# Kernel optimization log

Hardware: AMD Instinct MI355X
Metric: run time of the kernel (lower is better)

Reference implementation:

```python
import jax, jax.numpy as jnp
import numpy as np

EMBED_DIM = 1024
HEADS = 16
ATTN_NORM = 64  # scale divisor: score / sqrt(ATTN_NORM)


def setup_inputs() -> dict:
    key = jax.random.key(0)
    ks = jax.random.split(key, 12)
    B, S, E = 2, 2048, EMBED_DIM
    s = 1.0 / np.sqrt(E)
    inp = {
        "q": jax.random.normal(ks[0], (B, S, E), jnp.float32),
        "k": jax.random.normal(ks[1], (B, S, E), jnp.float32),
        "v": jax.random.normal(ks[2], (B, S, E), jnp.float32),
        "mask": jnp.zeros((B, 1, 1, S), dtype=bool),
        "Wq": jax.random.normal(ks[3], (E, E), jnp.float32) * s,
        "bq": jnp.zeros((E,), jnp.float32),
        "Wk": jax.random.normal(ks[4], (E, E), jnp.float32) * s,
        "bk": jnp.zeros((E,), jnp.float32),
        "Wv": jax.random.normal(ks[5], (E, E), jnp.float32) * s,
        "bv": jnp.zeros((E,), jnp.float32),
        "Wo": jax.random.normal(ks[6], (E, E), jnp.float32) * s,
        "bo": jnp.zeros((E,), jnp.float32),
    }
    return inp


def reference(q, k, v, mask, Wq, bq, Wk, bk, Wv, bv, Wo, bo):
    B, S, E = q.shape
    H = HEADS
    D = E // H
    residual = q
    # QKV projections (torch Linear: x @ W.T + b)
    qh = (q @ Wq.T + bq).reshape(B, S, H, D).transpose(0, 2, 1, 3)  # [B,H,S,D]
    kh = (k @ Wk.T + bk).reshape(B, S, H, D).transpose(0, 2, 1, 3)
    vh = (v @ Wv.T + bv).reshape(B, S, H, D).transpose(0, 2, 1, 3)
    # scaled dot-product attention with boolean mask -> -inf
    score = jnp.einsum("bhqd,bhkd->bhqk", qh, kh) / jnp.sqrt(jnp.asarray(ATTN_NORM, qh.dtype))
    score = jnp.where(mask, -jnp.inf, score)
    attn = jax.nn.softmax(score, axis=-1)
    out = jnp.einsum("bhqk,bhkd->bhqd", attn, vh)
    out = out.transpose(0, 2, 1, 3).reshape(B, S, E)
    # output projection + residual
    return out @ Wo.T + bo + residual
```

## Files before the change

kernel.cpp:

```cpp
#include <hip/hip_runtime.h>
#include <math.h>

typedef __bf16 bf16;
typedef __bf16 bf16x4 __attribute__((ext_vector_type(4)));
typedef __bf16 bf16x8 __attribute__((ext_vector_type(8)));
typedef float f32x4 __attribute__((ext_vector_type(4)));

typedef void __attribute__((address_space(1))) as1_void;
typedef void __attribute__((address_space(3))) as3_void;

__device__ __forceinline__ void async16(const void* g, void* l) {
  __builtin_amdgcn_global_load_lds((as1_void*)(void*)g, (as3_void*)l, 16, 0, 0);
}

__global__ void cast_all(const float* __restrict__ s0, const float* __restrict__ s1,
                         const float* __restrict__ s2, const float* __restrict__ s3,
                         const float* __restrict__ s4, const float* __restrict__ s5,
                         const float* __restrict__ s6, bf16* __restrict__ dst) {
  int i = blockIdx.x * 256 + threadIdx.x;
  const float* src; int base;
  if (i < 3145728) { int t = i >> 20; src = (t == 0) ? s0 : (t == 1 ? s1 : s2); base = t << 20; }
  else {
    int t = (i - 3145728) >> 18;
    src = (t == 0) ? s3 : (t == 1 ? s4 : (t == 2 ? s5 : s6));
    base = 3145728 + (t << 18);
  }
  float4 f = ((const float4*)src)[i - base];
  bf16x4 o; o[0] = (bf16)f.x; o[1] = (bf16)f.y; o[2] = (bf16)f.z; o[3] = (bf16)f.w;
  *(bf16x4*)(dst + (size_t)i * 4) = o;
}

template<int SWAP>
__device__ __forceinline__ void gemm_core(const bf16* __restrict__ A, const bf16* __restrict__ W,
                                          bf16* sA, bf16* sB, int m0, int n0, f32x4 acc[4][4]) {
  const int tid = threadIdx.x;
  const int wave = tid >> 6, lane = tid & 63, quad = lane >> 4, l16 = lane & 15;
  const int wm = (wave >> 1) * 64, wn = (wave & 1) * 64;
  for (int kt = 0; kt < 1024; kt += 64) {
    #pragma unroll
    for (int i = 0; i < 4; ++i) {
      int c = i * 256 + tid;
      int row = c >> 3, cg = c & 7;
      int gc = kt + ((cg ^ (row & 7)) << 3);
      async16(A + (size_t)(m0 + row) * 1024 + gc, (char*)sA + i * 4096 + wave * 1024);
      async16(W + (size_t)(n0 + row) * 1024 + gc, (char*)sB + i * 4096 + wave * 1024);
    }
    __syncthreads();
    #pragma unroll
    for (int kk = 0; kk < 2; ++kk) {
      bf16x8 af[4], bw[4];
      #pragma unroll
      for (int mi = 0; mi < 4; mi++) {
        int row = wm + mi * 16 + l16;
        af[mi] = *(const bf16x8*)&sA[row * 64 + (((quad + kk * 4) ^ (row & 7)) << 3)];
      }
      #pragma unroll
      for (int ni = 0; ni < 4; ni++) {
        int row = wn + ni * 16 + l16;
        bw[ni] = *(const bf16x8*)&sB[row * 64 + (((quad + kk * 4) ^ (row & 7)) << 3)];
      }
      #pragma unroll
      for (int mi = 0; mi < 4; mi++)
        #pragma unroll
        for (int ni = 0; ni < 4; ni++)
          acc[mi][ni] = SWAP
            ? __builtin_amdgcn_mfma_f32_16x16x32_bf16(bw[ni], af[mi], acc[mi][ni], 0, 0, 0)
            : __builtin_amdgcn_mfma_f32_16x16x32_bf16(af[mi], bw[ni], acc[mi][ni], 0, 0, 0);
    }
    __syncthreads();
  }
}

__global__ __launch_bounds__(256, 3)
void gemm_qkv(const bf16* __restrict__ A0, const bf16* __restrict__ A1, const bf16* __restrict__ A2,
              const bf16* __restrict__ W0, const bf16* __restrict__ W1, const bf16* __restrict__ W2,
              const float* __restrict__ b0, const float* __restrict__ b1, const float* __restrict__ b2,
              bf16* __restrict__ Qp, bf16* __restrict__ Kp, bf16* __restrict__ Vt) {
  __shared__ __align__(16) bf16 sA[128 * 64];
  __shared__ __align__(16) bf16 sB[128 * 64];
  const int z = blockIdx.z;
  const bf16* A = (z == 0) ? A0 : (z == 1 ? A1 : A2);
  const bf16* W = (z == 0) ? W0 : (z == 1 ? W1 : W2);
  const float* bias = (z == 0) ? b0 : (z == 1 ? b1 : b2);
  const int m0 = blockIdx.y * 128, n0 = blockIdx.x * 128;
  const int tid = threadIdx.x;
  const int wave = tid >> 6, lane = tid & 63, quad = lane >> 4, l16 = lane & 15;
  const int wm = (wave >> 1) * 64, wn = (wave & 1) * 64;

  f32x4 acc[4][4];
  #pragma unroll
  for (int mi = 0; mi < 4; mi++)
    #pragma unroll
    for (int ni = 0; ni < 4; ni++)
      #pragma unroll
      for (int r = 0; r < 4; r++) acc[mi][ni][r] = 0.f;

  if (z < 2) {
    gemm_core<1>(A, W, sA, sB, m0, n0, acc);
    bf16* out = (z == 0) ? Qp : Kp;
    const float sc = (z == 0) ? 0.125f : 1.0f;
    #pragma unroll
    for (int mi = 0; mi < 4; mi++) {
      int m = m0 + wm + mi * 16 + l16;
      #pragma unroll
      for (int ni = 0; ni < 4; ni++) {
        int nb = n0 + wn + ni * 16 + quad * 4;
        f32x4 b4 = *(const f32x4*)&bias[nb];
        bf16x4 o;
        #pragma unroll
        for (int r = 0; r < 4; r++) o[r] = (bf16)((acc[mi][ni][r] + b4[r]) * sc);
        *(bf16x4*)&out[(size_t)m * 1024 + nb] = o;
      }
    }
  } else {
    gemm_core<0>(A, W, sA, sB, m0, n0, acc);
    #pragma unroll
    for (int ni = 0; ni < 4; ni++) {
      int n_g = n0 + wn + ni * 16 + l16;
      float bs = bias[n_g];
      int h = n_g >> 6, d = n_g & 63;
      #pragma unroll
      for (int mi = 0; mi < 4; mi++) {
        int m_b = m0 + wm + mi * 16 + quad * 4;
        int b = m_b >> 11, s0 = m_b & 2047;
        bf16x4 o;
        #pragma unroll
        for (int r = 0; r < 4; r++) o[r] = (bf16)(acc[mi][ni][r] + bs);
        *(bf16x4*)&Vt[(size_t)((b * 16 + h) * 64 + d) * 2048 + s0] = o;
      }
    }
  }
}

__global__ __launch_bounds__(256, 2)
void gemm_o(const bf16* __restrict__ A, const bf16* __restrict__ W,
            const float* __restrict__ bias, const float* __restrict__ resid,
            float* __restrict__ out) {
  __shared__ __align__(16) bf16 sA[128 * 64];
  __shared__ __align__(16) bf16 sB[64 * 64];
  const int m0 = blockIdx.y * 128, n0 = blockIdx.x * 64;
  const int tid = threadIdx.x;
  const int wave = tid >> 6, lane = tid & 63, quad = lane >> 4, l16 = lane & 15;
  const int wm = (wave >> 1) * 64, wn = (wave & 1) * 32;

  f32x4 acc[4][2];
  #pragma unroll
  for (int mi = 0; mi < 4; mi++)
    #pragma unroll
    for (int ni = 0; ni < 2; ni++)
      #pragma unroll
      for (int r = 0; r < 4; r++) acc[mi][ni][r] = 0.f;

  for (int kt = 0; kt < 1024; kt += 64) {
    #pragma unroll
    for (int i = 0; i < 4; ++i) {
      int c = i * 256 + tid;
      int row = c >> 3, cg = c & 7;
      async16(A + (size_t)(m0 + row) * 1024 + kt + ((cg ^ (row & 7)) << 3),
              (char*)sA + i * 4096 + wave * 1024);
    }
    #pragma unroll
    for (int i = 0; i < 2; ++i) {
      int c = i * 256 + tid;
      int row = c >> 3, cg = c & 7;
      async16(W + (size_t)(n0 + row) * 1024 + kt + ((cg ^ (row & 7)) << 3),
              (char*)sB + i * 4096 + wave * 1024);
    }
    __syncthreads();
    #pragma unroll
    for (int kk = 0; kk < 2; ++kk) {
      bf16x8 af[4], bw[2];
      #pragma unroll
      for (int mi = 0; mi < 4; mi++) {
        int row = wm + mi * 16 + l16;
        af[mi] = *(const bf16x8*)&sA[row * 64 + (((quad + kk * 4) ^ (row & 7)) << 3)];
      }
      #pragma unroll
      for (int ni = 0; ni < 2; ni++) {
        int row = wn + ni * 16 + l16;
        bw[ni] = *(const bf16x8*)&sB[row * 64 + (((quad + kk * 4) ^ (row & 7)) << 3)];
      }
      #pragma unroll
      for (int mi = 0; mi < 4; mi++)
        #pragma unroll
        for (int ni = 0; ni < 2; ni++)
          acc[mi][ni] = __builtin_amdgcn_mfma_f32_16x16x32_bf16(bw[ni], af[mi], acc[mi][ni], 0, 0, 0);
    }
    __syncthreads();
  }
  #pragma unroll
  for (int mi = 0; mi < 4; mi++) {
    int m = m0 + wm + mi * 16 + l16;
    #pragma unroll
    for (int ni = 0; ni < 2; ni++) {
      int nb = n0 + wn + ni * 16 + quad * 4;
      f32x4 b4 = *(const f32x4*)&bias[nb];
      f32x4 r4 = *(const f32x4*)&resid[(size_t)m * 1024 + nb];
      f32x4 o;
      #pragma unroll
      for (int r = 0; r < 4; r++) o[r] = acc[mi][ni][r] + b4[r] + r4[r];
      *(f32x4*)&out[(size_t)m * 1024 + nb] = o;
    }
  }
}

__global__ __launch_bounds__(256, 2)
void attn_fused(const bf16* __restrict__ Qp, const bf16* __restrict__ Kp,
                const bf16* __restrict__ Vt, const unsigned char* __restrict__ mask,
                bf16* __restrict__ AO)
{
  __shared__ __align__(16) bf16 sK[128*64];
  __shared__ __align__(16) bf16 sV[64*128];
  __shared__ __align__(16) bf16 sP[128*136];
  const int tid  = threadIdx.x;
  const int wave = tid >> 6, lane = tid & 63, quad = lane >> 4, l16 = lane & 15;
  const int bh = blockIdx.x, qt = blockIdx.y;
  const int b = bh >> 4, h = bh & 15;
  const int q0 = qt * 128;
  const bf16* Kbase = Kp + (size_t)(b*2048)*1024 + h*64;
  const bf16* Vbase = Vt + (size_t)bh*64*2048;

  bf16x8 aq[2][2];
  #pragma unroll
  for (int qg = 0; qg < 2; qg++) {
    const bf16* Qrow = Qp + (size_t)(b*2048 + q0 + (wave*2+qg)*16 + l16)*1024 + h*64;
    aq[qg][0] = *(const bf16x8*)(Qrow + quad*8);
    aq[qg][1] = *(const bf16x8*)(Qrow + 32 + quad*8);
  }

  auto stageKV = [&](int kt) {
    int k0 = kt * 128;
    #pragma unroll
    for (int i = 0; i < 4; i++) {
      int c = i*256 + tid;
      int rk = c >> 3, cgk = c & 7;
      async16(Kbase + (size_t)(k0 + rk)*1024 + ((cgk ^ (rk & 7)) << 3),
              (char*)sK + i*4096 + wave*1024);
      int d = c >> 4, cgv = c & 15;
      async16(Vbase + (size_t)d*2048 + k0 + ((cgv ^ (d & 15)) << 3),
              (char*)sV + i*4096 + wave*1024);
    }
  };

  float l_lane[2] = {0.f, 0.f};
  f32x4 oacc[2][4];
  #pragma unroll
  for (int qg = 0; qg < 2; qg++)
    #pragma unroll
    for (int ni = 0; ni < 4; ni++)
      #pragma unroll
      for (int r = 0; r < 4; r++) oacc[qg][ni][r] = 0.f;

  bf16* pb[2] = { &sP[(wave*2 + 0)*16*136], &sP[(wave*2 + 1)*16*136] };
  stageKV(0);

  const float L2E = 1.44269504f;
  for (int kt = 0; kt < 16; ++kt) {
    __syncthreads();
    f32x4 sacc[2][8];
    #pragma unroll
    for (int qg = 0; qg < 2; qg++)
      #pragma unroll
      for (int ni = 0; ni < 8; ni++)
        #pragma unroll
        for (int r = 0; r < 4; r++) sacc[qg][ni][r] = 0.f;
    #pragma unroll
    for (int ks = 0; ks < 2; ks++)
      #pragma unroll
      for (int ni = 0; ni < 8; ni++) {
        int rk = ni*16 + l16;
        bf16x8 bk = *(const bf16x8*)&sK[rk*64 + (((quad + ks*4) ^ (rk & 7)) << 3)];
        sacc[0][ni] = __builtin_amdgcn_mfma_f32_16x16x32_bf16(bk, aq[0][ks], sacc[0][ni], 0, 0, 0);
        sacc[1][ni] = __builtin_amdgcn_mfma_f32_16x16x32_bf16(bk, aq[1][ks], sacc[1][ni], 0, 0, 0);
      }
    int mbase = b*2048 + kt*128;
    unsigned mw = ((const unsigned*)(mask + mbase))[lane & 31];
    if (__any(mw != 0)) {
      #pragma unroll
      for (int ni = 0; ni < 8; ni++) {
        unsigned mk = *(const unsigned*)&mask[mbase + ni*16 + quad*4];
        #pragma unroll
        for (int r = 0; r < 4; r++)
          if ((mk >> (8*r)) & 0xff) { sacc[0][ni][r] = -1e30f; sacc[1][ni][r] = -1e30f; }
      }
    }
    #pragma unroll
    for (int qg = 0; qg < 2; qg++) {
      float rs = 0.f;
      #pragma unroll
      for (int ni = 0; ni < 8; ni++)
        #pragma unroll
        for (int r = 0; r < 4; r++) {
          float p = __builtin_amdgcn_exp2f(sacc[qg][ni][r] * L2E);
          sacc[qg][ni][r] = p;
          rs += p;
        }
      l_lane[qg] += rs;
      #pragma unroll
      for (int ni = 0; ni < 8; ni++) {
        bf16x4 pw;
        #pragma unroll
        for (int r = 0; r < 4; r++) pw[r] = (bf16)sacc[qg][ni][r];
        *(bf16x4*)&pb[qg][l16*136 + ni*16 + quad*4] = pw;
      }
    }
    #pragma unroll
    for (int ks = 0; ks < 4; ks++) {
      bf16x8 pf0 = *(const bf16x8*)&pb[0][l16*136 + ks*32 + quad*8];
      bf16x8 pf1 = *(const bf16x8*)&pb[1][l16*136 + ks*32 + quad*8];
      #pragma unroll
      for (int ni = 0; ni < 4; ni++) {
        int d = ni*16 + l16;
        bf16x8 av = *(const bf16x8*)&sV[d*128 + (((ks*4 + quad) ^ (d & 15)) << 3)];
        oacc[0][ni] = __builtin_amdgcn_mfma_f32_16x16x32_bf16(av, pf0, oacc[0][ni], 0, 0, 0);
        oacc[1][ni] = __builtin_amdgcn_mfma_f32_16x16x32_bf16(av, pf1, oacc[1][ni], 0, 0, 0);
      }
    }
    __syncthreads();
    if (kt < 15) stageKV(kt + 1);
  }

  #pragma unroll
  for (int qg = 0; qg < 2; qg++) {
    float l = l_lane[qg];
    l += __shfl_xor(l, 16);
    l += __shfl_xor(l, 32);
    float inv = 1.0f / l;
    int s = q0 + (wave*2 + qg)*16 + l16;
    #pragma unroll
    for (int ni = 0; ni < 4; ni++) {
      bf16x4 o;
      #pragma unroll
      for (int r = 0; r < 4; r++) o[r] = (bf16)(oacc[qg][ni][r] * inv);
      *(bf16x4*)&AO[(size_t)(b*2048 + s)*1024 + h*64 + ni*16 + quad*4] = o;
    }
  }
}

extern "C" void kernel_launch(void* const* d_in, const int* in_sizes, int n_in,
                              void* d_out, int out_size, void* d_ws, size_t ws_size,
                              hipStream_t stream) {
  (void)in_sizes; (void)n_in; (void)out_size; (void)ws_size;
  const float* qf = (const float*)d_in[0];
  const float* kf = (const float*)d_in[1];
  const float* vf = (const float*)d_in[2];
  const unsigned char* mask = (const unsigned char*)d_in[3];
  const float* Wq = (const float*)d_in[4];
  const float* bq = (const float*)d_in[5];
  const float* Wk = (const float*)d_in[6];
  const float* bk = (const float*)d_in[7];
  const float* Wv = (const float*)d_in[8];
  const float* bv = (const float*)d_in[9];
  const float* Wo = (const float*)d_in[10];
  const float* bo = (const float*)d_in[11];

  bf16* p = (bf16*)d_ws;
  bf16* Qb  = p; p += 4194304;
  bf16* Kb  = p; p += 4194304;
  bf16* Vb  = p; p += 4194304;
  bf16* Wqb = p; p += 1048576;
  bf16* Wkb = p; p += 1048576;
  bf16* Wvb = p; p += 1048576;
  bf16* Wob = p; p += 1048576;
  bf16* Qp  = p; p += 4194304;
  bf16* Kp  = p; p += 4194304;
  bf16* Vtp = p; p += 4194304;
  bf16* AO  = p; p += 4194304;

  cast_all<<<16384, 256, 0, stream>>>(qf, kf, vf, Wq, Wk, Wv, Wo, Qb);
  gemm_qkv<<<dim3(8, 32, 3), 256, 0, stream>>>(Qb, Kb, Vb, Wqb, Wkb, Wvb,
                                               bq, bk, bv, Qp, Kp, Vtp);
  attn_fused<<<dim3(32, 16), 256, 0, stream>>>(Qp, Kp, Vtp, mask, AO);
  gemm_o<<<dim3(16, 32), 256, 0, stream>>>(AO, Wob, bo, qf, (float*)d_out);
}
```

Measured before the change: 223.1 us.

## Rewrite attention with 32x32 MFMA, register-resident P and double-buffered K/V

```diff
diff --git a/kernel.cpp b/kernel.cpp
--- a/kernel.cpp
+++ b/kernel.cpp
@@ -5,6 +5,7 @@
 typedef __bf16 bf16x4 __attribute__((ext_vector_type(4)));
 typedef __bf16 bf16x8 __attribute__((ext_vector_type(8)));
 typedef float f32x4 __attribute__((ext_vector_type(4)));
+typedef float f32x16 __attribute__((ext_vector_type(16)));
 
 typedef void __attribute__((address_space(1))) as1_void;
 typedef void __attribute__((address_space(3))) as3_void;
@@ -123,10 +124,13 @@
       for (int mi = 0; mi < 4; mi++) {
         int m_b = m0 + wm + mi * 16 + quad * 4;
         int b = m_b >> 11, s0 = m_b & 2047;
+        int sp = s0 & 15;
+        int spp = (sp == 4) ? 8 : ((sp == 8) ? 4 : sp);
+        int s1 = (s0 & ~15) | spp;
         bf16x4 o;
         #pragma unroll
         for (int r = 0; r < 4; r++) o[r] = (bf16)(acc[mi][ni][r] + bs);
-        *(bf16x4*)&Vt[(size_t)((b * 16 + h) * 64 + d) * 2048 + s0] = o;
+        *(bf16x4*)&Vt[(size_t)((b * 16 + h) * 64 + d) * 2048 + s1] = o;
       }
     }
   }
@@ -204,136 +208,148 @@
   }
 }
 
-__global__ __launch_bounds__(256, 2)
+__global__ __launch_bounds__(256, 1)
 void attn_fused(const bf16* __restrict__ Qp, const bf16* __restrict__ Kp,
                 const bf16* __restrict__ Vt, const unsigned char* __restrict__ mask,
                 bf16* __restrict__ AO)
 {
-  __shared__ __align__(16) bf16 sK[128*64];
-  __shared__ __align__(16) bf16 sV[64*128];
-  __shared__ __align__(16) bf16 sP[128*136];
-  const int tid  = threadIdx.x;
-  const int wave = tid >> 6, lane = tid & 63, quad = lane >> 4, l16 = lane & 15;
+  __shared__ __align__(16) bf16 sK[2 * 128 * 64];
+  __shared__ __align__(16) bf16 sV[2 * 64 * 128];
+  const int tid = threadIdx.x;
+  const int wave = tid >> 6, lane = tid & 63, l31 = lane & 31, hl = lane >> 5;
   const int bh = blockIdx.x, qt = blockIdx.y;
   const int b = bh >> 4, h = bh & 15;
-  const int q0 = qt * 128;
-  const bf16* Kbase = Kp + (size_t)(b*2048)*1024 + h*64;
-  const bf16* Vbase = Vt + (size_t)bh*64*2048;
-
-  bf16x8 aq[2][2];
+  const int q0 = qt * 256;
+  const bf16* Kbase = Kp + (size_t)(b * 2048) * 1024 + h * 64;
+  const bf16* Vbase = Vt + (size_t)bh * 64 * 2048;
+
+  bf16x8 qf[2][4];
   #pragma unroll
   for (int qg = 0; qg < 2; qg++) {
-    const bf16* Qrow = Qp + (size_t)(b*2048 + q0 + (wave*2+qg)*16 + l16)*1024 + h*64;
-    aq[qg][0] = *(const bf16x8*)(Qrow + quad*8);
-    aq[qg][1] = *(const bf16x8*)(Qrow + 32 + quad*8);
-  }
-
-  auto stageKV = [&](int kt) {
+    const bf16* Qrow = Qp + (size_t)(b * 2048 + q0 + wave * 64 + qg * 32 + l31) * 1024 + h * 64;
+    #pragma unroll
+    for (int ks = 0; ks < 4; ks++)
+      qf[qg][ks] = *(const bf16x8*)(Qrow + ks * 16 + hl * 8);
+  }
+
+  unsigned mor = 0;
+  #pragma unroll
+  for (int i = 0; i < 8; i++)
+    mor |= ((const unsigned*)(mask + b * 2048))[lane + i * 64];
+  const bool anymask = __any(mor != 0);
+
+  auto stageKV = [&](int kt, int buf) {
     int k0 = kt * 128;
+    char* dK = (char*)sK + buf * 16384;
+    char* dV = (char*)sV + buf * 16384;
     #pragma unroll
     for (int i = 0; i < 4; i++) {
-      int c = i*256 + tid;
+      int c = i * 256 + tid;
       int rk = c >> 3, cgk = c & 7;
-      async16(Kbase + (size_t)(k0 + rk)*1024 + ((cgk ^ (rk & 7)) << 3),
-              (char*)sK + i*4096 + wave*1024);
+      async16(Kbase + (size_t)(k0 + rk) * 1024 + ((cgk ^ (rk & 7)) << 3),
+              dK + i * 4096 + wave * 1024);
       int d = c >> 4, cgv = c & 15;
-      async16(Vbase + (size_t)d*2048 + k0 + ((cgv ^ (d & 15)) << 3),
-              (char*)sV + i*4096 + wave*1024);
+      async16(Vbase + (size_t)d * 2048 + k0 + ((cgv ^ (d & 15)) << 3),
+              dV + i * 4096 + wave * 1024);
     }
   };
 
   float l_lane[2] = {0.f, 0.f};
-  f32x4 oacc[2][4];
+  f32x16 oacc[2][2];
   #pragma unroll
   for (int qg = 0; qg < 2; qg++)
     #pragma unroll
-    for (int ni = 0; ni < 4; ni++)
-      #pragma unroll
-      for (int r = 0; r < 4; r++) oacc[qg][ni][r] = 0.f;
-
-  bf16* pb[2] = { &sP[(wave*2 + 0)*16*136], &sP[(wave*2 + 1)*16*136] };
-  stageKV(0);
-
+    for (int db = 0; db < 2; db++)
+      #pragma unroll
+      for (int r = 0; r < 16; r++) oacc[qg][db][r] = 0.f;
+
+  stageKV(0, 0);
   const float L2E = 1.44269504f;
+
   for (int kt = 0; kt < 16; ++kt) {
-    __syncthreads();
-    f32x4 sacc[2][8];
+    int buf = kt & 1;
+    __syncthreads();
+    if (kt < 15) stageKV(kt + 1, buf ^ 1);
+    const bf16* kbuf = sK + buf * 8192;
+    const bf16* vbuf = sV + buf * 8192;
+
+    f32x16 sacc[2][4];
     #pragma unroll
     for (int qg = 0; qg < 2; qg++)
       #pragma unroll
-      for (int ni = 0; ni < 8; ni++)
-        #pragma unroll
-        for (int r = 0; r < 4; r++) sacc[qg][ni][r] = 0.f;
-    #pragma unroll
-    for (int ks = 0; ks < 2; ks++)
-      #pragma unroll
-      for (int ni = 0; ni < 8; ni++) {
-        int rk = ni*16 + l16;
-        bf16x8 bk = *(const bf16x8*)&sK[rk*64 + (((quad + ks*4) ^ (rk & 7)) << 3)];
-        sacc[0][ni] = __builtin_amdgcn_mfma_f32_16x16x32_bf16(bk, aq[0][ks], sacc[0][ni], 0, 0, 0);
-        sacc[1][ni] = __builtin_amdgcn_mfma_f32_16x16x32_bf16(bk, aq[1][ks], sacc[1][ni], 0, 0, 0);
-      }
-    int mbase = b*2048 + kt*128;
-    unsigned mw = ((const unsigned*)(mask + mbase))[lane & 31];
-    if (__any(mw != 0)) {
-      #pragma unroll
-      for (int ni = 0; ni < 8; ni++) {
-        unsigned mk = *(const unsigned*)&mask[mbase + ni*16 + quad*4];
-        #pragma unroll
-        for (int r = 0; r < 4; r++)
-          if ((mk >> (8*r)) & 0xff) { sacc[0][ni][r] = -1e30f; sacc[1][ni][r] = -1e30f; }
-      }
-    }
+      for (int kb = 0; kb < 4; kb++)
+        #pragma unroll
+        for (int r = 0; r < 16; r++) sacc[qg][kb][r] = 0.f;
+    #pragma unroll
+    for (int ks = 0; ks < 4; ks++)
+      #pragma unroll
+      for (int kb = 0; kb < 4; kb++) {
+        bf16x8 ak = *(const bf16x8*)&kbuf[(kb * 32 + l31) * 64 + (((2 * ks + hl) ^ (l31 & 7)) << 3)];
+        sacc[0][kb] = __builtin_amdgcn_mfma_f32_32x32x16_bf16(ak, qf[0][ks], sacc[0][kb], 0, 0, 0);
+        sacc[1][kb] = __builtin_amdgcn_mfma_f32_32x32x16_bf16(ak, qf[1][ks], sacc[1][kb], 0, 0, 0);
+      }
+
+    if (anymask) {
+      int mbase = b * 2048 + kt * 128;
+      #pragma unroll
+      for (int kb = 0; kb < 4; kb++)
+        #pragma unroll
+        for (int g2 = 0; g2 < 4; g2++) {
+          unsigned m4 = *(const unsigned*)&mask[mbase + kb * 32 + g2 * 8 + hl * 4];
+          #pragma unroll
+          for (int rr = 0; rr < 4; rr++)
+            if ((m4 >> (8 * rr)) & 0xff) {
+              sacc[0][kb][g2 * 4 + rr] = -1e30f;
+              sacc[1][kb][g2 * 4 + rr] = -1e30f;
+            }
+        }
+    }
+
+    bf16x8 pfrag[2][4][2];
     #pragma unroll
     for (int qg = 0; qg < 2; qg++) {
       float rs = 0.f;
       #pragma unroll
-      for (int ni = 0; ni < 8; ni++)
-        #pragma unroll
-        for (int r = 0; r < 4; r++) {
-          float p = __builtin_amdgcn_exp2f(sacc[qg][ni][r] * L2E);
-          sacc[qg][ni][r] = p;
-          rs += p;
+      for (int kb = 0; kb < 4; kb++)
+        #pragma unroll
+        for (int s = 0; s < 2; s++)
+          #pragma unroll
+          for (int j = 0; j < 8; j++) {
+            float p = __builtin_amdgcn_exp2f(sacc[qg][kb][8 * s + j] * L2E);
+            rs += p;
+            pfrag[qg][kb][s][j] = (bf16)p;
+          }
+      l_lane[qg] += rs;
+    }
+
+    #pragma unroll
+    for (int kb = 0; kb < 4; kb++)
+      #pragma unroll
+      for (int s = 0; s < 2; s++) {
+        int g = kb * 2 + s;
+        #pragma unroll
+        for (int db = 0; db < 2; db++) {
+          bf16x8 av = *(const bf16x8*)&vbuf[(db * 32 + l31) * 128 + (((2 * g + hl) ^ (l31 & 15)) << 3)];
+          oacc[0][db] = __builtin_amdgcn_mfma_f32_32x32x16_bf16(av, pfrag[0][kb][s], oacc[0][db], 0, 0, 0);
+          oacc[1][db] = __builtin_amdgcn_mfma_f32_32x32x16_bf16(av, pfrag[1][kb][s], oacc[1][db], 0, 0, 0);
         }
-      l_lane[qg] += rs;
-      #pragma unroll
-      for (int ni = 0; ni < 8; ni++) {
-        bf16x4 pw;
-        #pragma unroll
-        for (int r = 0; r < 4; r++) pw[r] = (bf16)sacc[qg][ni][r];
-        *(bf16x4*)&pb[qg][l16*136 + ni*16 + quad*4] = pw;
-      }
-    }
-    #pragma unroll
-    for (int ks = 0; ks < 4; ks++) {
-      bf16x8 pf0 = *(const bf16x8*)&pb[0][l16*136 + ks*32 + quad*8];
-      bf16x8 pf1 = *(const bf16x8*)&pb[1][l16*136 + ks*32 + quad*8];
-      #pragma unroll
-      for (int ni = 0; ni < 4; ni++) {
-        int d = ni*16 + l16;
-        bf16x8 av = *(const bf16x8*)&sV[d*128 + (((ks*4 + quad) ^ (d & 15)) << 3)];
-        oacc[0][ni] = __builtin_amdgcn_mfma_f32_16x16x32_bf16(av, pf0, oacc[0][ni], 0, 0, 0);
-        oacc[1][ni] = __builtin_amdgcn_mfma_f32_16x16x32_bf16(av, pf1, oacc[1][ni], 0, 0, 0);
-      }
-    }
-    __syncthreads();
-    if (kt < 15) stageKV(kt + 1);
+      }
   }
 
   #pragma unroll
   for (int qg = 0; qg < 2; qg++) {
-    float l = l_lane[qg];
-    l += __shfl_xor(l, 16);
-    l += __shfl_xor(l, 32);
+    float l = l_lane[qg] + __shfl_xor(l_lane[qg], 32);
     float inv = 1.0f / l;
-    int s = q0 + (wave*2 + qg)*16 + l16;
-    #pragma unroll
-    for (int ni = 0; ni < 4; ni++) {
-      bf16x4 o;
-      #pragma unroll
-      for (int r = 0; r < 4; r++) o[r] = (bf16)(oacc[qg][ni][r] * inv);
-      *(bf16x4*)&AO[(size_t)(b*2048 + s)*1024 + h*64 + ni*16 + quad*4] = o;
-    }
+    int s = q0 + wave * 64 + qg * 32 + l31;
+    #pragma unroll
+    for (int db = 0; db < 2; db++)
+      #pragma unroll
+      for (int g2 = 0; g2 < 4; g2++) {
+        bf16x4 o;
+        #pragma unroll
+        for (int r = 0; r < 4; r++) o[r] = (bf16)(oacc[qg][db][g2 * 4 + r] * inv);
+        *(bf16x4*)&AO[(size_t)(b * 2048 + s) * 1024 + h * 64 + db * 32 + g2 * 8 + hl * 4] = o;
+      }
   }
 }
 
@@ -370,6 +386,6 @@
   cast_all<<<16384, 256, 0, stream>>>(qf, kf, vf, Wq, Wk, Wv, Wo, Qb);
   gemm_qkv<<<dim3(8, 32, 3), 256, 0, stream>>>(Qb, Kb, Vb, Wqb, Wkb, Wvb,
                                                bq, bk, bv, Qp, Kp, Vtp);
-  attn_fused<<<dim3(32, 16), 256, 0, stream>>>(Qp, Kp, Vtp, mask, AO);
+  attn_fused<<<dim3(32, 8), 256, 0, stream>>>(Qp, Kp, Vtp, mask, AO);
   gemm_o<<<dim3(16, 32), 256, 0, stream>>>(AO, Wob, bo, qf, (float*)d_out);
 }
```

Result: slower. 230.0 us (+3.1%).
